# Kernel optimization log

Hardware: AMD Instinct MI355X
Metric: run time of the kernel (lower is better)

Reference implementation:

```python
import jax, jax.numpy as jnp
import numpy as np

N_HEAD = 12
NEG = 1e9


def setup_inputs() -> dict:
    key = jax.random.key(0)
    k1, k2, k3 = jax.random.split(key, 3)
    B, S, D = 1, 4096, 768
    x = jax.random.normal(k1, (B, S, D), dtype=jnp.float32)
    w_attn = jax.random.normal(k2, (D, 3 * D), dtype=jnp.float32) * 0.02
    b_attn = jnp.zeros((3 * D,), dtype=jnp.float32)
    w_proj = jax.random.normal(k3, (D, D), dtype=jnp.float32) * 0.02
    b_proj = jnp.zeros((D,), dtype=jnp.float32)
    return {"x": x, "w_attn": w_attn, "b_attn": b_attn, "w_proj": w_proj, "b_proj": b_proj}


def reference(x, w_attn, b_attn, w_proj, b_proj):
    B, S, D = x.shape
    H = N_HEAD
    hd = D // H
    qkv = x @ w_attn + b_attn  # [B,S,3D]
    q, k, v = jnp.split(qkv, 3, axis=-1)
    # split heads -> [B,H,S,hd]
    q = q.reshape(B, S, H, hd).transpose(0, 2, 1, 3)
    k = k.reshape(B, S, H, hd).transpose(0, 2, 1, 3)
    v = v.reshape(B, S, H, hd).transpose(0, 2, 1, 3)
    w = jnp.einsum('bhqd,bhkd->bhqk', q, k) / jnp.sqrt(jnp.float32(hd))
    mask = jnp.tril(jnp.ones((S, S), dtype=w.dtype))  # causal tril buffer
    w = w * mask - NEG * (1.0 - mask)
    w = jax.nn.softmax(w, axis=-1)
    a = jnp.einsum('bhqk,bhkd->bhqd', w, v)
    a = a.transpose(0, 2, 1, 3).reshape(B, S, D)  # merge heads
    return a @ w_proj + b_proj
```

## Files before the change

kernel.cpp:

```cpp
#include <hip/hip_runtime.h>

typedef __bf16 bf16x8 __attribute__((ext_vector_type(8)));
typedef float f32x4 __attribute__((ext_vector_type(4)));
typedef float f32x16 __attribute__((ext_vector_type(16)));
typedef unsigned short u16;

__device__ inline u16 f2bf(float f) {
  union { float f; unsigned int u; } v; v.f = f;
  unsigned int r = v.u + 0x7fffu + ((v.u >> 16) & 1u);
  return (u16)(r >> 16);
}

__device__ inline void load_lds16(const void* g, void* l) {
  __builtin_amdgcn_global_load_lds((const __attribute__((address_space(1))) unsigned int*)g,
                                   (__attribute__((address_space(3))) unsigned int*)l, 16, 0, 0);
}

__global__ __launch_bounds__(256) void prep(const float* __restrict__ x,
                                            const float* __restrict__ w_attn,
                                            const float* __restrict__ w_proj,
                                            u16* __restrict__ xb, u16* __restrict__ wTa,
                                            u16* __restrict__ wTp) {
  const int b = blockIdx.x;
  const int tid = threadIdx.x;
  if (b < 3072) {
    const int i = b * 1024 + tid * 4;
    float4 v = *(const float4*)(x + i);
    ushort4 o;
    o.x = f2bf(v.x); o.y = f2bf(v.y); o.z = f2bf(v.z); o.w = f2bf(v.w);
    *(ushort4*)(xb + i) = o;
    return;
  }
  __shared__ float tile[32][33];
  const float* in;
  u16* out;
  int R, C, c0, r0;
  if (b < 4800) {
    const int b2 = b - 3072;
    in = w_attn; out = wTa; R = 768; C = 2304;
    c0 = (b2 % 72) * 32; r0 = (b2 / 72) * 32;
  } else {
    const int b3 = b - 4800;
    in = w_proj; out = wTp; R = 768; C = 768;
    c0 = (b3 % 24) * 32; r0 = (b3 / 24) * 32;
  }
  const int tx = tid & 31, ty = tid >> 5;
#pragma unroll
  for (int i = ty; i < 32; i += 8)
    tile[i][tx] = in[(size_t)(r0 + i) * C + c0 + tx];
  __syncthreads();
#pragma unroll
  for (int i = ty; i < 32; i += 8)
    out[(size_t)(c0 + i) * R + r0 + tx] = f2bf(tile[tx][i]);
}

__global__ __launch_bounds__(256) void vtrans(const u16* __restrict__ qkv, u16* __restrict__ vT) {
  const int h = blockIdx.y;
  const int s0 = blockIdx.x * 64;
  const int tid = threadIdx.x;
  __shared__ u16 T[64][72];
  {
    const int key = tid >> 2, dq = (tid & 3) * 16;
    const u16* g = qkv + (size_t)(s0 + key) * 2304 + 1536 + h * 64 + dq;
    *(uint4*)&T[key][dq] = *(const uint4*)g;
    *(uint4*)&T[key][dq + 8] = *(const uint4*)(g + 8);
  }
  __syncthreads();
  {
    const int d = tid >> 2, sq = (tid & 3) * 16;
    u16 tmp[16];
#pragma unroll
    for (int e = 0; e < 16; ++e) tmp[e] = T[sq + e][d];
    u16* o = vT + ((size_t)h * 64 + d) * 4096 + s0 + sq;
    *(uint4*)o = *(uint4*)tmp;
    *(uint4*)(o + 8) = *(uint4*)(tmp + 8);
  }
}

template <int BF16_OUT>
__global__ __launch_bounds__(256) void gemm_bt(const u16* __restrict__ A, const u16* __restrict__ BT,
                                               const float* __restrict__ bias, void* __restrict__ Cv,
                                               int M, int N, int K, int nx) {
  __shared__ __align__(16) u16 As[128 * 32];
  __shared__ __align__(16) u16 Bs[128 * 32];
  const int tid = threadIdx.x;
  const int wave = tid >> 6, lane = tid & 63;
  const int g = lane >> 4, lr = lane & 15;
  const int bid = blockIdx.x;
  const int swz = (bid & 7) * ((int)gridDim.x >> 3) + (bid >> 3);
  const int m0 = (swz / nx) * 128, n0 = (swz % nx) * 128;
  const int wr = (wave >> 1) * 64, wc = (wave & 1) * 64;
  f32x4 acc[4][4] = {};

  for (int k0 = 0; k0 < K; k0 += 32) {
    __syncthreads();
#pragma unroll
    for (int j = 0; j < 2; ++j) {
      const int e = tid * 8 + j * 2048;
      const int r = e >> 5, c = e & 31;
      const u16* ga = A + (size_t)(m0 + r) * K + k0 + c;
      const u16* gb = BT + (size_t)(n0 + r) * K + k0 + c;
      load_lds16(ga, (void*)(As + wave * 512 + j * 2048));
      load_lds16(gb, (void*)(Bs + wave * 512 + j * 2048));
    }
    __syncthreads();
    const u16* pa = As + (wr + lr) * 32 + g * 8;
    const u16* pb = Bs + (wc + lr) * 32 + g * 8;
    bf16x8 a[4], b[4];
#pragma unroll
    for (int i = 0; i < 4; ++i) a[i] = *(const bf16x8*)(pa + i * 16 * 32);
#pragma unroll
    for (int j = 0; j < 4; ++j) b[j] = *(const bf16x8*)(pb + j * 16 * 32);
#pragma unroll
    for (int i = 0; i < 4; ++i)
#pragma unroll
      for (int j = 0; j < 4; ++j)
        acc[i][j] = __builtin_amdgcn_mfma_f32_16x16x32_bf16(a[i], b[j], acc[i][j], 0, 0, 0);
  }

#pragma unroll
  for (int i = 0; i < 4; ++i)
#pragma unroll
    for (int j = 0; j < 4; ++j)
#pragma unroll
      for (int r = 0; r < 4; ++r) {
        int row = m0 + wr + i * 16 + g * 4 + r;
        int col = n0 + wc + j * 16 + lr;
        float v = acc[i][j][r] + bias[col];
        if (BF16_OUT)
          ((u16*)Cv)[(size_t)row * N + col] = f2bf(v);
        else
          ((float*)Cv)[(size_t)row * N + col] = v;
      }
}

#define MNEG 30000.0f
template <int CH, int DIRECT>
__global__ __launch_bounds__(256, 3) void attn(const u16* __restrict__ qkv, const u16* __restrict__ vT,
                                               u16* __restrict__ pO, float* __restrict__ pml,
                                               u16* __restrict__ aout) {
  __shared__ __align__(16) u16 KV[4][4096];

  const int bid = blockIdx.x;
  const int h = bid % 12;
  int g, c;
  if (DIRECT) {
    g = 31 - bid / 12;
    c = 0;
  } else {
    const int u = 79 - bid / 12;
    if (u < 8) { g = u; c = 0; }
    else if (u < 24) { g = 8 + ((u - 8) >> 1); c = (u - 8) & 1; }
    else if (u < 48) { g = 16 + (u - 24) / 3; c = (u - 24) % 3; }
    else { g = 24 + ((u - 48) >> 2); c = (u - 48) & 3; }
  }

  const int tid = threadIdx.x;
  const int wave = tid >> 6;
  const int l = tid & 63;
  const int lr = l & 31;
  const int H = l >> 5;
  const int H4 = H * 4, H8 = H * 8;

  const int qt = 4 * g + wave;
  const int q0 = qt * 32;
  const int nkt = (qt >> 1) + 1;
  const int t0 = DIRECT ? 0 : c * CH;
  const int tend = min(2 * g + 2, t0 + CH);

  const u16* kgb = qkv + 768 + h * 64;
  const u16* vgb = vT + (size_t)h * 64 * 4096;

  const int srow = l >> 3;
  int kSo[2], vSo[2];
#pragma unroll
  for (int i = 0; i < 2; ++i) {
    const int row = 16 * wave + 8 * i + srow;
    const int sc = ((l & 7) ^ srow ^ (2 * wave + i)) << 3;
    kSo[i] = row * 2304 + sc;
    vSo[i] = row * 4096 + sc;
  }

  const u16* Rd[2][4];
#pragma unroll
  for (int b2 = 0; b2 < 2; ++b2) {
    const int row = 32 * b2 + lr;
    const int sw = (row ^ (row >> 3)) & 7;
#pragma unroll
    for (int cc = 0; cc < 4; ++cc)
      Rd[b2][cc] = &KV[0][row * 64 + (((2 * cc + H) ^ sw) << 3)];
  }

  bf16x8 qB[4];
  {
    const u16* qp = qkv + (size_t)(q0 + lr) * 2304 + h * 64;
    const float qs = 0.125f * 1.4426950408889634f;
#pragma unroll
    for (int cc = 0; cc < 4; ++cc) {
      bf16x8 raw = *(const bf16x8*)(qp + 16 * cc + H8);
#pragma unroll
      for (int e = 0; e < 8; ++e) qB[cc][e] = (__bf16)((float)raw[e] * qs);
    }
  }

  f32x16 O[2] = {};
  float mst = -MNEG, lst = 0.f;

#define STAGE(T, BUF)                                                      \
  {                                                                        \
    const size_t kk = (size_t)(T) * 64;                                    \
    _Pragma("unroll") for (int i = 0; i < 2; ++i) {                        \
      load_lds16(kgb + kk * 2304 + kSo[i], &KV[(BUF)][(2 * wave + i) * 512]); \
      load_lds16(vgb + kk + vSo[i], &KV[2 + (BUF)][(2 * wave + i) * 512]); \
    }                                                                      \
  }

#define BODY(T, BUF)                                                                        \
  {                                                                                         \
    if ((T) + 1 < tend) {                                                                   \
      STAGE((T) + 1, (BUF) ^ 1);                                                            \
      asm volatile("s_waitcnt vmcnt(4)" ::: "memory");                                      \
    } else {                                                                                \
      asm volatile("s_waitcnt vmcnt(0)" ::: "memory");                                      \
    }                                                                                       \
    __builtin_amdgcn_s_barrier();                                                           \
    __builtin_amdgcn_sched_barrier(0);                                                      \
    f32x16 s[2] = {};                                                                       \
    _Pragma("unroll") for (int kb = 0; kb < 2; ++kb)                                        \
      _Pragma("unroll") for (int cc = 0; cc < 4; ++cc) {                                    \
        bf16x8 kf = *(const bf16x8*)(Rd[kb][cc] + (BUF) * 4096);                            \
        s[kb] = __builtin_amdgcn_mfma_f32_32x32x16_bf16(kf, qB[cc], s[kb], 0, 0, 0);        \
      }                                                                                     \
    bf16x8 vf[2][4];                                                                        \
    _Pragma("unroll") for (int da = 0; da < 2; ++da)                                        \
      _Pragma("unroll") for (int cc = 0; cc < 4; ++cc)                                      \
        vf[da][cc] = *(const bf16x8*)(Rd[da][cc] + 8192 + (BUF) * 4096);                    \
    if ((T) >= nkt - 1) {                                                                   \
      const int rel = q0 + lr - (T) * 64;                                                   \
      _Pragma("unroll") for (int kb = 0; kb < 2; ++kb)                                      \
        _Pragma("unroll") for (int r = 0; r < 16; ++r)                                      \
          if (32 * kb + (r & 3) + 8 * (r >> 2) + H4 > rel) s[kb][r] = -MNEG;                \
    }                                                                                       \
    float mx = s[0][0];                                                                     \
    _Pragma("unroll") for (int kb = 0; kb < 2; ++kb)                                        \
      _Pragma("unroll") for (int r = 0; r < 16; ++r) mx = fmaxf(mx, s[kb][r]);              \
    mx = fmaxf(mx, __shfl_xor(mx, 32));                                                     \
    if (__any(mx > mst + 12.f)) {                                                           \
      const float mn = fmaxf(mst, mx);                                                      \
      const float alpha = __builtin_amdgcn_exp2f(mst - mn);                                 \
      mst = mn;                                                                             \
      lst *= alpha;                                                                         \
      O[0] *= alpha;                                                                        \
      O[1] *= alpha;                                                                        \
    }                                                                                       \
    float rs = 0.f;                                                                         \
    _Pragma("unroll") for (int kb = 0; kb < 2; ++kb)                                        \
      _Pragma("unroll") for (int r = 0; r < 16; ++r) {                                      \
        const float p = __builtin_amdgcn_exp2f(s[kb][r] - mst);                             \
        s[kb][r] = p;                                                                       \
        rs += p;                                                                            \
      }                                                                                     \
    rs += __shfl_xor(rs, 32);                                                               \
    lst += rs;                                                                              \
    unsigned w[16];                                                                         \
    _Pragma("unroll") for (int kb = 0; kb < 2; ++kb)                                        \
      _Pragma("unroll") for (int j2 = 0; j2 < 4; ++j2) {                                    \
        asm("v_cvt_pk_bf16_f32 %0, %1, %2"                                                  \
            : "=v"(w[kb * 8 + j2 * 2]) : "v"(s[kb][4 * j2]), "v"(s[kb][4 * j2 + 1]));       \
        asm("v_cvt_pk_bf16_f32 %0, %1, %2"                                                  \
            : "=v"(w[kb * 8 + j2 * 2 + 1]) : "v"(s[kb][4 * j2 + 2]), "v"(s[kb][4 * j2 + 3])); \
      }                                                                                     \
    unsigned recv[8];                                                                       \
    _Pragma("unroll") for (int cc = 0; cc < 4; ++cc)                                        \
      _Pragma("unroll") for (int m = 0; m < 2; ++m) {                                       \
        const unsigned send = H ? w[4 * cc + m] : w[4 * cc + 2 + m];                        \
        recv[cc * 2 + m] = (unsigned)__shfl_xor((int)send, 32);                             \
      }                                                                                     \
    _Pragma("unroll") for (int cc = 0; cc < 4; ++cc) {                                      \
      union { unsigned u[4]; bf16x8 v; } Bp;                                                \
      Bp.u[0] = H ? recv[2 * cc] : w[4 * cc];                                               \
      Bp.u[1] = H ? recv[2 * cc + 1] : w[4 * cc + 1];                                       \
      Bp.u[2] = H ? w[4 * cc + 2] : recv[2 * cc];                                           \
      Bp.u[3] = H ? w[4 * cc + 3] : recv[2 * cc + 1];                                       \
      O[0] = __builtin_amdgcn_mfma_f32_32x32x16_bf16(vf[0][cc], Bp.v, O[0], 0, 0, 0);       \
      O[1] = __builtin_amdgcn_mfma_f32_32x32x16_bf16(vf[1][cc], Bp.v, O[1], 0, 0, 0);       \
    }                                                                                       \
    __builtin_amdgcn_s_barrier();                                                           \
  }

  STAGE(t0, 0);
  int t = t0;
  for (; t + 2 <= tend; t += 2) {
    BODY(t, 0);
    BODY(t + 1, 1);
  }
  if (t < tend) BODY(t, 0);
#undef BODY
#undef STAGE

  if (DIRECT) {
    const float inv = 1.0f / lst;
    u16* orow = aout + (size_t)(q0 + lr) * 768 + h * 64;
#pragma unroll
    for (int da = 0; da < 2; ++da)
#pragma unroll
      for (int j2 = 0; j2 < 4; ++j2) {
        ushort4 st;
        st.x = f2bf(O[da][4 * j2 + 0] * inv);
        st.y = f2bf(O[da][4 * j2 + 1] * inv);
        st.z = f2bf(O[da][4 * j2 + 2] * inv);
        st.w = f2bf(O[da][4 * j2 + 3] * inv);
        *(ushort4*)(orow + 32 * da + 8 * j2 + H4) = st;
      }
  } else {
    const int slot = (h * 128 + qt) * 4 + c;
    u16* po = pO + (size_t)slot * 2048 + lr * 64;
#pragma unroll
    for (int da = 0; da < 2; ++da)
#pragma unroll
      for (int j2 = 0; j2 < 4; ++j2) {
        ushort4 st;
        st.x = f2bf(O[da][4 * j2 + 0]);
        st.y = f2bf(O[da][4 * j2 + 1]);
        st.z = f2bf(O[da][4 * j2 + 2]);
        st.w = f2bf(O[da][4 * j2 + 3]);
        *(ushort4*)(po + 32 * da + 8 * j2 + H4) = st;
      }
    if (H == 0) {
      float2 ml; ml.x = mst; ml.y = lst;
      *(float2*)(pml + (size_t)slot * 64 + lr * 2) = ml;
    }
  }
}

__global__ __launch_bounds__(64) void combine(const u16* __restrict__ pO, const float* __restrict__ pml,
                                              u16* __restrict__ aout, int ncmax, int CHv) {
  const int bid = blockIdx.x;
  const int h = bid % 12, qt = bid / 12;
  const int nkt = (qt >> 1) + 1;
  const int nc = (nkt + CHv - 1) / CHv;
  const int sb = (h * 128 + qt) * ncmax;
  const int t = threadIdx.x;
  const int row = t & 31, H = t >> 5;

  float m[4], lw[4];
  float M = -__builtin_inff();
#pragma unroll
  for (int c = 0; c < 4; ++c)
    if (c < nc) {
      m[c] = pml[(size_t)(sb + c) * 64 + row * 2];
      M = fmaxf(M, m[c]);
    }
  float L = 0.f;
#pragma unroll
  for (int c = 0; c < 4; ++c)
    if (c < nc) {
      lw[c] = __builtin_amdgcn_exp2f(m[c] - M);
      L += pml[(size_t)(sb + c) * 64 + row * 2 + 1] * lw[c];
    }

  float acc[32] = {};
#pragma unroll
  for (int c = 0; c < 4; ++c)
    if (c < nc) {
      const u16* p = pO + (size_t)(sb + c) * 2048 + row * 64 + 32 * H;
      const float wgt = lw[c];
#pragma unroll
      for (int k = 0; k < 4; ++k) {
        bf16x8 v = *(const bf16x8*)(p + 8 * k);
#pragma unroll
        for (int e = 0; e < 8; ++e) acc[k * 8 + e] += (float)v[e] * wgt;
      }
    }

  const float inv = 1.0f / L;
  u16 ov[32];
#pragma unroll
  for (int d = 0; d < 32; ++d) ov[d] = f2bf(acc[d] * inv);
  u16* dst = aout + (size_t)(qt * 32 + row) * 768 + h * 64 + 32 * H;
#pragma unroll
  for (int k = 0; k < 4; ++k) *(uint4*)(dst + 8 * k) = *(const uint4*)(ov + 8 * k);
}

extern "C" void kernel_launch(void* const* d_in, const int* in_sizes, int n_in,
                              void* d_out, int out_size, void* d_ws, size_t ws_size,
                              hipStream_t stream) {
  const float* x = (const float*)d_in[0];
  const float* w_attn = (const float*)d_in[1];
  const float* b_attn = (const float*)d_in[2];
  const float* w_proj = (const float*)d_in[3];
  const float* b_proj = (const float*)d_in[4];
  float* out = (float*)d_out;

  const int S = 4096, D = 768;
  u16* xb = (u16*)d_ws;
  u16* wTa = xb + (size_t)S * D;
  u16* wTp = wTa + (size_t)3 * D * D;
  u16* qkv = wTp + (size_t)D * D;
  u16* abuf = qkv + (size_t)S * 3 * D;
  u16* vTb = abuf + (size_t)S * D;
  u16* pO = vTb + (size_t)12 * 64 * 4096;

  const size_t base_bytes = (size_t)(3145728 + 1769472 + 589824 + 9437184 + 3145728 + 3145728) * 2;
  const size_t need16 = base_bytes + (size_t)6144 * 2048 * 2 + (size_t)6144 * 64 * 4;

  prep<<<dim3(5376), 256, 0, stream>>>(x, w_attn, w_proj, xb, wTa, wTp);
  gemm_bt<1><<<dim3(576), 256, 0, stream>>>(xb, wTa, b_attn, qkv, S, 3 * D, D, 18);
  vtrans<<<dim3(S / 64, 12), 256, 0, stream>>>(qkv, vTb);

  if (ws_size >= need16) {
    float* pml = (float*)(pO + (size_t)6144 * 2048);
    attn<16, 0><<<dim3(12 * 80), 256, 0, stream>>>(qkv, vTb, pO, pml, abuf);
    combine<<<dim3(12 * 128), 64, 0, stream>>>(pO, pml, abuf, 4, 16);
  } else {
    attn<64, 1><<<dim3(12 * 32), 256, 0, stream>>>(qkv, vTb, abuf, (float*)abuf, abuf);
  }

  gemm_bt<0><<<dim3(192), 256, 0, stream>>>(abuf, wTp, b_proj, out, S, D, D, 6);
}
```

Before: 135.4 us.

## Make split-KV attention persistent with atomic work queue and MFMA priority hints

```diff
diff --git a/kernel.cpp b/kernel.cpp
--- a/kernel.cpp
+++ b/kernel.cpp
@@ -135,25 +135,11 @@
 }
 
 #define MNEG 30000.0f
-template <int CH, int DIRECT>
-__global__ __launch_bounds__(256, 3) void attn(const u16* __restrict__ qkv, const u16* __restrict__ vT,
-                                               u16* __restrict__ pO, float* __restrict__ pml,
-                                               u16* __restrict__ aout) {
+__global__ __launch_bounds__(256, 3) void attn_p(const u16* __restrict__ qkv, const u16* __restrict__ vT,
+                                                 u16* __restrict__ pO, float* __restrict__ pml,
+                                                 int* __restrict__ ctr) {
   __shared__ __align__(16) u16 KV[4][4096];
-
-  const int bid = blockIdx.x;
-  const int h = bid % 12;
-  int g, c;
-  if (DIRECT) {
-    g = 31 - bid / 12;
-    c = 0;
-  } else {
-    const int u = 79 - bid / 12;
-    if (u < 8) { g = u; c = 0; }
-    else if (u < 24) { g = 8 + ((u - 8) >> 1); c = (u - 8) & 1; }
-    else if (u < 48) { g = 16 + (u - 24) / 3; c = (u - 24) % 3; }
-    else { g = 24 + ((u - 48) >> 2); c = (u - 48) & 3; }
-  }
+  __shared__ int unit_s;
 
   const int tid = threadIdx.x;
   const int wave = tid >> 6;
@@ -162,15 +148,6 @@
   const int H = l >> 5;
   const int H4 = H * 4, H8 = H * 8;
 
-  const int qt = 4 * g + wave;
-  const int q0 = qt * 32;
-  const int nkt = (qt >> 1) + 1;
-  const int t0 = DIRECT ? 0 : c * CH;
-  const int tend = min(2 * g + 2, t0 + CH);
-
-  const u16* kgb = qkv + 768 + h * 64;
-  const u16* vgb = vT + (size_t)h * 64 * 4096;
-
   const int srow = l >> 3;
   int kSo[2], vSo[2];
 #pragma unroll
@@ -180,7 +157,6 @@
     kSo[i] = row * 2304 + sc;
     vSo[i] = row * 4096 + sc;
   }
-
   const u16* Rd[2][4];
 #pragma unroll
   for (int b2 = 0; b2 < 2; ++b2) {
@@ -191,28 +167,51 @@
       Rd[b2][cc] = &KV[0][row * 64 + (((2 * cc + H) ^ sw) << 3)];
   }
 
-  bf16x8 qB[4];
-  {
-    const u16* qp = qkv + (size_t)(q0 + lr) * 2304 + h * 64;
-    const float qs = 0.125f * 1.4426950408889634f;
-#pragma unroll
-    for (int cc = 0; cc < 4; ++cc) {
-      bf16x8 raw = *(const bf16x8*)(qp + 16 * cc + H8);
-#pragma unroll
-      for (int e = 0; e < 8; ++e) qB[cc][e] = (__bf16)((float)raw[e] * qs);
-    }
-  }
-
-  f32x16 O[2] = {};
-  float mst = -MNEG, lst = 0.f;
-
-#define STAGE(T, BUF)                                                      \
-  {                                                                        \
-    const size_t kk = (size_t)(T) * 64;                                    \
-    _Pragma("unroll") for (int i = 0; i < 2; ++i) {                        \
+  while (true) {
+    if (tid == 0) unit_s = atomicAdd(ctr, 1);
+    __syncthreads();
+    const int unit = unit_s;
+    if (unit >= 960) break;
+
+    const int h = unit % 12;
+    const int u = 79 - unit / 12;
+    int g, c;
+    if (u < 8) { g = u; c = 0; }
+    else if (u < 24) { g = 8 + ((u - 8) >> 1); c = (u - 8) & 1; }
+    else if (u < 48) { g = 16 + (u - 24) / 3; c = (u - 24) % 3; }
+    else { g = 24 + ((u - 48) >> 2); c = (u - 48) & 3; }
+
+    const int qt = 4 * g + wave;
+    const int q0 = qt * 32;
+    const int nkt = (qt >> 1) + 1;
+    const int t0 = c * 16;
+    const int tend = min(2 * g + 2, t0 + 16);
+
+    const u16* kgb = qkv + 768 + h * 64;
+    const u16* vgb = vT + (size_t)h * 64 * 4096;
+
+    bf16x8 qB[4];
+    {
+      const u16* qp = qkv + (size_t)(q0 + lr) * 2304 + h * 64;
+      const float qs = 0.125f * 1.4426950408889634f;
+#pragma unroll
+      for (int cc = 0; cc < 4; ++cc) {
+        bf16x8 raw = *(const bf16x8*)(qp + 16 * cc + H8);
+#pragma unroll
+        for (int e = 0; e < 8; ++e) qB[cc][e] = (__bf16)((float)raw[e] * qs);
+      }
+    }
+
+    f32x16 O[2] = {};
+    float mst = -MNEG, lst = 0.f;
+
+#define STAGE(T, BUF)                                                         \
+  {                                                                           \
+    const size_t kk = (size_t)(T) * 64;                                       \
+    _Pragma("unroll") for (int i = 0; i < 2; ++i) {                           \
       load_lds16(kgb + kk * 2304 + kSo[i], &KV[(BUF)][(2 * wave + i) * 512]); \
-      load_lds16(vgb + kk + vSo[i], &KV[2 + (BUF)][(2 * wave + i) * 512]); \
-    }                                                                      \
+      load_lds16(vgb + kk + vSo[i], &KV[2 + (BUF)][(2 * wave + i) * 512]);    \
+    }                                                                         \
   }
 
 #define BODY(T, BUF)                                                                        \
@@ -226,11 +225,13 @@
     __builtin_amdgcn_s_barrier();                                                           \
     __builtin_amdgcn_sched_barrier(0);                                                      \
     f32x16 s[2] = {};                                                                       \
+    __builtin_amdgcn_s_setprio(1);                                                          \
     _Pragma("unroll") for (int kb = 0; kb < 2; ++kb)                                        \
       _Pragma("unroll") for (int cc = 0; cc < 4; ++cc) {                                    \
         bf16x8 kf = *(const bf16x8*)(Rd[kb][cc] + (BUF) * 4096);                            \
         s[kb] = __builtin_amdgcn_mfma_f32_32x32x16_bf16(kf, qB[cc], s[kb], 0, 0, 0);        \
       }                                                                                     \
+    __builtin_amdgcn_s_setprio(0);                                                          \
     bf16x8 vf[2][4];                                                                        \
     _Pragma("unroll") for (int da = 0; da < 2; ++da)                                        \
       _Pragma("unroll") for (int cc = 0; cc < 4; ++cc)                                      \
@@ -276,6 +277,7 @@
         const unsigned send = H ? w[4 * cc + m] : w[4 * cc + 2 + m];                        \
         recv[cc * 2 + m] = (unsigned)__shfl_xor((int)send, 32);                             \
       }                                                                                     \
+    __builtin_amdgcn_s_setprio(1);                                                          \
     _Pragma("unroll") for (int cc = 0; cc < 4; ++cc) {                                      \
       union { unsigned u[4]; bf16x8 v; } Bp;                                                \
       Bp.u[0] = H ? recv[2 * cc] : w[4 * cc];                                               \
@@ -285,34 +287,20 @@
       O[0] = __builtin_amdgcn_mfma_f32_32x32x16_bf16(vf[0][cc], Bp.v, O[0], 0, 0, 0);       \
       O[1] = __builtin_amdgcn_mfma_f32_32x32x16_bf16(vf[1][cc], Bp.v, O[1], 0, 0, 0);       \
     }                                                                                       \
+    __builtin_amdgcn_s_setprio(0);                                                          \
     __builtin_amdgcn_s_barrier();                                                           \
   }
 
-  STAGE(t0, 0);
-  int t = t0;
-  for (; t + 2 <= tend; t += 2) {
-    BODY(t, 0);
-    BODY(t + 1, 1);
-  }
-  if (t < tend) BODY(t, 0);
+    STAGE(t0, 0);
+    int t = t0;
+    for (; t + 2 <= tend; t += 2) {
+      BODY(t, 0);
+      BODY(t + 1, 1);
+    }
+    if (t < tend) BODY(t, 0);
 #undef BODY
 #undef STAGE
 
-  if (DIRECT) {
-    const float inv = 1.0f / lst;
-    u16* orow = aout + (size_t)(q0 + lr) * 768 + h * 64;
-#pragma unroll
-    for (int da = 0; da < 2; ++da)
-#pragma unroll
-      for (int j2 = 0; j2 < 4; ++j2) {
-        ushort4 st;
-        st.x = f2bf(O[da][4 * j2 + 0] * inv);
-        st.y = f2bf(O[da][4 * j2 + 1] * inv);
-        st.z = f2bf(O[da][4 * j2 + 2] * inv);
-        st.w = f2bf(O[da][4 * j2 + 3] * inv);
-        *(ushort4*)(orow + 32 * da + 8 * j2 + H4) = st;
-      }
-  } else {
     const int slot = (h * 128 + qt) * 4 + c;
     u16* po = pO + (size_t)slot * 2048 + lr * 64;
 #pragma unroll
@@ -333,6 +321,162 @@
   }
 }
 
+template <int CH, int DIRECT>
+__global__ __launch_bounds__(256, 3) void attn(const u16* __restrict__ qkv, const u16* __restrict__ vT,
+                                               u16* __restrict__ pO, float* __restrict__ pml,
+                                               u16* __restrict__ aout) {
+  __shared__ __align__(16) u16 KV[4][4096];
+  const int bid = blockIdx.x;
+  const int h = bid % 12;
+  int g = 31 - bid / 12, c = 0;
+  const int tid = threadIdx.x;
+  const int wave = tid >> 6;
+  const int l = tid & 63;
+  const int lr = l & 31;
+  const int H = l >> 5;
+  const int H4 = H * 4, H8 = H * 8;
+  const int qt = 4 * g + wave;
+  const int q0 = qt * 32;
+  const int nkt = (qt >> 1) + 1;
+  const int t0 = 0;
+  const int tend = min(2 * g + 2, t0 + CH);
+  const u16* kgb = qkv + 768 + h * 64;
+  const u16* vgb = vT + (size_t)h * 64 * 4096;
+  const int srow = l >> 3;
+  int kSo[2], vSo[2];
+#pragma unroll
+  for (int i = 0; i < 2; ++i) {
+    const int row = 16 * wave + 8 * i + srow;
+    const int sc = ((l & 7) ^ srow ^ (2 * wave + i)) << 3;
+    kSo[i] = row * 2304 + sc;
+    vSo[i] = row * 4096 + sc;
+  }
+  const u16* Rd[2][4];
+#pragma unroll
+  for (int b2 = 0; b2 < 2; ++b2) {
+    const int row = 32 * b2 + lr;
+    const int sw = (row ^ (row >> 3)) & 7;
+#pragma unroll
+    for (int cc = 0; cc < 4; ++cc)
+      Rd[b2][cc] = &KV[0][row * 64 + (((2 * cc + H) ^ sw) << 3)];
+  }
+  bf16x8 qB[4];
+  {
+    const u16* qp = qkv + (size_t)(q0 + lr) * 2304 + h * 64;
+    const float qs = 0.125f * 1.4426950408889634f;
+#pragma unroll
+    for (int cc = 0; cc < 4; ++cc) {
+      bf16x8 raw = *(const bf16x8*)(qp + 16 * cc + H8);
+#pragma unroll
+      for (int e = 0; e < 8; ++e) qB[cc][e] = (__bf16)((float)raw[e] * qs);
+    }
+  }
+  f32x16 O[2] = {};
+  float mst = -MNEG, lst = 0.f;
+#define STAGE(T, BUF)                                                         \
+  {                                                                           \
+    const size_t kk = (size_t)(T) * 64;                                       \
+    _Pragma("unroll") for (int i = 0; i < 2; ++i) {                           \
+      load_lds16(kgb + kk * 2304 + kSo[i], &KV[(BUF)][(2 * wave + i) * 512]); \
+      load_lds16(vgb + kk + vSo[i], &KV[2 + (BUF)][(2 * wave + i) * 512]);    \
+    }                                                                         \
+  }
+#define BODY(T, BUF)                                                                        \
+  {                                                                                         \
+    if ((T) + 1 < tend) {                                                                   \
+      STAGE((T) + 1, (BUF) ^ 1);                                                            \
+      asm volatile("s_waitcnt vmcnt(4)" ::: "memory");                                      \
+    } else {                                                                                \
+      asm volatile("s_waitcnt vmcnt(0)" ::: "memory");                                      \
+    }                                                                                       \
+    __builtin_amdgcn_s_barrier();                                                           \
+    __builtin_amdgcn_sched_barrier(0);                                                      \
+    f32x16 s[2] = {};                                                                       \
+    _Pragma("unroll") for (int kb = 0; kb < 2; ++kb)                                        \
+      _Pragma("unroll") for (int cc = 0; cc < 4; ++cc) {                                    \
+        bf16x8 kf = *(const bf16x8*)(Rd[kb][cc] + (BUF) * 4096);                            \
+        s[kb] = __builtin_amdgcn_mfma_f32_32x32x16_bf16(kf, qB[cc], s[kb], 0, 0, 0);        \
+      }                                                                                     \
+    bf16x8 vf[2][4];                                                                        \
+    _Pragma("unroll") for (int da = 0; da < 2; ++da)                                        \
+      _Pragma("unroll") for (int cc = 0; cc < 4; ++cc)                                      \
+        vf[da][cc] = *(const bf16x8*)(Rd[da][cc] + 8192 + (BUF) * 4096);                    \
+    if ((T) >= nkt - 1) {                                                                   \
+      const int rel = q0 + lr - (T) * 64;                                                   \
+      _Pragma("unroll") for (int kb = 0; kb < 2; ++kb)                                      \
+        _Pragma("unroll") for (int r = 0; r < 16; ++r)                                      \
+          if (32 * kb + (r & 3) + 8 * (r >> 2) + H4 > rel) s[kb][r] = -MNEG;                \
+    }                                                                                       \
+    float mx = s[0][0];                                                                     \
+    _Pragma("unroll") for (int kb = 0; kb < 2; ++kb)                                        \
+      _Pragma("unroll") for (int r = 0; r < 16; ++r) mx = fmaxf(mx, s[kb][r]);              \
+    mx = fmaxf(mx, __shfl_xor(mx, 32));                                                     \
+    if (__any(mx > mst + 12.f)) {                                                           \
+      const float mn = fmaxf(mst, mx);                                                      \
+      const float alpha = __builtin_amdgcn_exp2f(mst - mn);                                 \
+      mst = mn;                                                                             \
+      lst *= alpha;                                                                         \
+      O[0] *= alpha;                                                                        \
+      O[1] *= alpha;                                                                        \
+    }                                                                                       \
+    float rs = 0.f;                                                                         \
+    _Pragma("unroll") for (int kb = 0; kb < 2; ++kb)                                        \
+      _Pragma("unroll") for (int r = 0; r < 16; ++r) {                                      \
+        const float p = __builtin_amdgcn_exp2f(s[kb][r] - mst);                             \
+        s[kb][r] = p;                                                                       \
+        rs += p;                                                                            \
+      }                                                                                     \
+    rs += __shfl_xor(rs, 32);                                                               \
+    lst += rs;                                                                              \
+    unsigned w[16];                                                                         \
+    _Pragma("unroll") for (int kb = 0; kb < 2; ++kb)                                        \
+      _Pragma("unroll") for (int j2 = 0; j2 < 4; ++j2) {                                    \
+        asm("v_cvt_pk_bf16_f32 %0, %1, %2"                                                  \
+            : "=v"(w[kb * 8 + j2 * 2]) : "v"(s[kb][4 * j2]), "v"(s[kb][4 * j2 + 1]));       \
+        asm("v_cvt_pk_bf16_f32 %0, %1, %2"                                                  \
+            : "=v"(w[kb * 8 + j2 * 2 + 1]) : "v"(s[kb][4 * j2 + 2]), "v"(s[kb][4 * j2 + 3])); \
+      }                                                                                     \
+    unsigned recv[8];                                                                       \
+    _Pragma("unroll") for (int cc = 0; cc < 4; ++cc)                                        \
+      _Pragma("unroll") for (int m = 0; m < 2; ++m) {                                       \
+        const unsigned send = H ? w[4 * cc + m] : w[4 * cc + 2 + m];                        \
+        recv[cc * 2 + m] = (unsigned)__shfl_xor((int)send, 32);                             \
+      }                                                                                     \
+    _Pragma("unroll") for (int cc = 0; cc < 4; ++cc) {                                      \
+      union { unsigned u[4]; bf16x8 v; } Bp;                                                \
+      Bp.u[0] = H ? recv[2 * cc] : w[4 * cc];                                               \
+      Bp.u[1] = H ? recv[2 * cc + 1] : w[4 * cc + 1];                                       \
+      Bp.u[2] = H ? w[4 * cc + 2] : recv[2 * cc];                                           \
+      Bp.u[3] = H ? w[4 * cc + 3] : recv[2 * cc + 1];                                       \
+      O[0] = __builtin_amdgcn_mfma_f32_32x32x16_bf16(vf[0][cc], Bp.v, O[0], 0, 0, 0);       \
+      O[1] = __builtin_amdgcn_mfma_f32_32x32x16_bf16(vf[1][cc], Bp.v, O[1], 0, 0, 0);       \
+    }                                                                                       \
+    __builtin_amdgcn_s_barrier();                                                           \
+  }
+  STAGE(t0, 0);
+  int t = t0;
+  for (; t + 2 <= tend; t += 2) {
+    BODY(t, 0);
+    BODY(t + 1, 1);
+  }
+  if (t < tend) BODY(t, 0);
+#undef BODY
+#undef STAGE
+  const float inv = 1.0f / lst;
+  u16* orow = aout + (size_t)(q0 + lr) * 768 + h * 64;
+#pragma unroll
+  for (int da = 0; da < 2; ++da)
+#pragma unroll
+    for (int j2 = 0; j2 < 4; ++j2) {
+      ushort4 st;
+      st.x = f2bf(O[da][4 * j2 + 0] * inv);
+      st.y = f2bf(O[da][4 * j2 + 1] * inv);
+      st.z = f2bf(O[da][4 * j2 + 2] * inv);
+      st.w = f2bf(O[da][4 * j2 + 3] * inv);
+      *(ushort4*)(orow + 32 * da + 8 * j2 + H4) = st;
+    }
+}
+
 __global__ __launch_bounds__(64) void combine(const u16* __restrict__ pO, const float* __restrict__ pml,
                                               u16* __restrict__ aout, int ncmax, int CHv) {
   const int bid = blockIdx.x;
@@ -402,7 +546,7 @@
   u16* pO = vTb + (size_t)12 * 64 * 4096;
 
   const size_t base_bytes = (size_t)(3145728 + 1769472 + 589824 + 9437184 + 3145728 + 3145728) * 2;
-  const size_t need16 = base_bytes + (size_t)6144 * 2048 * 2 + (size_t)6144 * 64 * 4;
+  const size_t need16 = base_bytes + (size_t)6144 * 2048 * 2 + (size_t)6144 * 64 * 4 + 64;
 
   prep<<<dim3(5376), 256, 0, stream>>>(x, w_attn, w_proj, xb, wTa, wTp);
   gemm_bt<1><<<dim3(576), 256, 0, stream>>>(xb, wTa, b_attn, qkv, S, 3 * D, D, 18);
@@ -410,7 +554,9 @@
 
   if (ws_size >= need16) {
     float* pml = (float*)(pO + (size_t)6144 * 2048);
-    attn<16, 0><<<dim3(12 * 80), 256, 0, stream>>>(qkv, vTb, pO, pml, abuf);
+    int* ctr = (int*)(pml + (size_t)6144 * 64);
+    hipMemsetAsync(ctr, 0, 4, stream);
+    attn_p<<<dim3(768), 256, 0, stream>>>(qkv, vTb, pO, pml, ctr);
     combine<<<dim3(12 * 128), 64, 0, stream>>>(pO, pml, abuf, 4, 16);
   } else {
     attn<64, 1><<<dim3(12 * 32), 256, 0, stream>>>(qkv, vTb, abuf, (float*)abuf, abuf);
```

After: 156.9 us. +15.9%, slower.

## Fuse V transpose into QKV GEMM epilogue and skip combine for single-chunk tiles

Applied to the files above, without the earlier changes.

```diff
diff --git a/kernel.cpp b/kernel.cpp
--- a/kernel.cpp
+++ b/kernel.cpp
@@ -54,32 +54,10 @@
     out[(size_t)(c0 + i) * R + r0 + tx] = f2bf(tile[tx][i]);
 }
 
-__global__ __launch_bounds__(256) void vtrans(const u16* __restrict__ qkv, u16* __restrict__ vT) {
-  const int h = blockIdx.y;
-  const int s0 = blockIdx.x * 64;
-  const int tid = threadIdx.x;
-  __shared__ u16 T[64][72];
-  {
-    const int key = tid >> 2, dq = (tid & 3) * 16;
-    const u16* g = qkv + (size_t)(s0 + key) * 2304 + 1536 + h * 64 + dq;
-    *(uint4*)&T[key][dq] = *(const uint4*)g;
-    *(uint4*)&T[key][dq + 8] = *(const uint4*)(g + 8);
-  }
-  __syncthreads();
-  {
-    const int d = tid >> 2, sq = (tid & 3) * 16;
-    u16 tmp[16];
-#pragma unroll
-    for (int e = 0; e < 16; ++e) tmp[e] = T[sq + e][d];
-    u16* o = vT + ((size_t)h * 64 + d) * 4096 + s0 + sq;
-    *(uint4*)o = *(uint4*)tmp;
-    *(uint4*)(o + 8) = *(uint4*)(tmp + 8);
-  }
-}
-
 template <int BF16_OUT>
 __global__ __launch_bounds__(256) void gemm_bt(const u16* __restrict__ A, const u16* __restrict__ BT,
                                                const float* __restrict__ bias, void* __restrict__ Cv,
+                                               u16* __restrict__ vT,
                                                int M, int N, int K, int nx) {
   __shared__ __align__(16) u16 As[128 * 32];
   __shared__ __align__(16) u16 Bs[128 * 32];
@@ -116,6 +94,24 @@
 #pragma unroll
       for (int j = 0; j < 4; ++j)
         acc[i][j] = __builtin_amdgcn_mfma_f32_16x16x32_bf16(a[i], b[j], acc[i][j], 0, 0, 0);
+  }
+
+  if (BF16_OUT && n0 >= 1536) {
+#pragma unroll
+    for (int i = 0; i < 4; ++i)
+#pragma unroll
+      for (int j = 0; j < 4; ++j) {
+        const int row = m0 + wr + i * 16 + g * 4;
+        const int col = n0 + wc + j * 16 + lr;
+        const float bb = bias[col];
+        ushort4 st;
+        st.x = f2bf(acc[i][j][0] + bb);
+        st.y = f2bf(acc[i][j][1] + bb);
+        st.z = f2bf(acc[i][j][2] + bb);
+        st.w = f2bf(acc[i][j][3] + bb);
+        *(ushort4*)(vT + (size_t)(col - 1536) * 4096 + row) = st;
+      }
+    return;
   }
 
 #pragma unroll
@@ -298,7 +294,7 @@
 #undef BODY
 #undef STAGE
 
-  if (DIRECT) {
+  if (DIRECT || g < 8) {
     const float inv = 1.0f / lst;
     u16* orow = aout + (size_t)(q0 + lr) * 768 + h * 64;
 #pragma unroll
@@ -336,7 +332,7 @@
 __global__ __launch_bounds__(64) void combine(const u16* __restrict__ pO, const float* __restrict__ pml,
                                               u16* __restrict__ aout, int ncmax, int CHv) {
   const int bid = blockIdx.x;
-  const int h = bid % 12, qt = bid / 12;
+  const int h = bid % 12, qt = 32 + bid / 12;
   const int nkt = (qt >> 1) + 1;
   const int nc = (nkt + CHv - 1) / CHv;
   const int sb = (h * 128 + qt) * ncmax;
@@ -405,16 +401,15 @@
   const size_t need16 = base_bytes + (size_t)6144 * 2048 * 2 + (size_t)6144 * 64 * 4;
 
   prep<<<dim3(5376), 256, 0, stream>>>(x, w_attn, w_proj, xb, wTa, wTp);
-  gemm_bt<1><<<dim3(576), 256, 0, stream>>>(xb, wTa, b_attn, qkv, S, 3 * D, D, 18);
-  vtrans<<<dim3(S / 64, 12), 256, 0, stream>>>(qkv, vTb);
+  gemm_bt<1><<<dim3(576), 256, 0, stream>>>(xb, wTa, b_attn, qkv, vTb, S, 3 * D, D, 18);
 
   if (ws_size >= need16) {
     float* pml = (float*)(pO + (size_t)6144 * 2048);
     attn<16, 0><<<dim3(12 * 80), 256, 0, stream>>>(qkv, vTb, pO, pml, abuf);
-    combine<<<dim3(12 * 128), 64, 0, stream>>>(pO, pml, abuf, 4, 16);
+    combine<<<dim3(12 * 96), 64, 0, stream>>>(pO, pml, abuf, 4, 16);
   } else {
     attn<64, 1><<<dim3(12 * 32), 256, 0, stream>>>(qkv, vTb, abuf, (float*)abuf, abuf);
   }
 
-  gemm_bt<0><<<dim3(192), 256, 0, stream>>>(abuf, wTp, b_proj, out, S, D, D, 6);
-}
+  gemm_bt<0><<<dim3(192), 256, 0, stream>>>(abuf, wTp, b_proj, out, (u16*)nullptr, S, D, D, 6);
+}
```

Result: slower. 145.6 us (+7.5%).
